# Kernel optimization log

Hardware: AMD Instinct MI355X
Metric: run time of the kernel (lower is better)

The kernel has to match this reference:

```python
import jax, jax.numpy as jnp
import numpy as np

H = 256          # hidden_channels
R = 64           # num_rbf
N = 20000        # nodes
E = 320000       # edges
CUTOFF_LO = 0.0
CUTOFF_UP = 5.0
LN_EPS = 1e-5


def _layernorm(x, g, b):
    mu = jnp.mean(x, axis=-1, keepdims=True)
    var = jnp.var(x, axis=-1, keepdims=True)
    return (x - mu) * jax.lax.rsqrt(var + LN_EPS) * g + b


def _cosine_cutoff(r):
    # cutoff_lower == 0 branch of CosineCutoff
    c = 0.5 * (jnp.cos(r * (jnp.pi / CUTOFF_UP)) + 1.0)
    return c * (r < CUTOFF_UP).astype(r.dtype)


def setup_inputs() -> dict:
    key = jax.random.key(0)
    ks = jax.random.split(key, 16)
    def xavier(k, shape):
        fan_in, fan_out = shape[1], shape[0]
        lim = np.sqrt(6.0 / (fan_in + fan_out))
        return jax.random.uniform(k, shape, jnp.float32, -lim, lim)
    x = jax.random.normal(ks[0], (N, H), jnp.float32)
    edge_index = jax.random.randint(ks[1], (2, E), 0, N, jnp.int64)
    edge_weight = jax.random.uniform(ks[2], (E,), jnp.float32, 0.0, CUTOFF_UP)
    edge_attr = jax.random.normal(ks[3], (E, R), jnp.float32)
    return {
        "x": x,
        "edge_index": edge_index,
        "edge_weight": edge_weight,
        "edge_attr": edge_attr,
        "ln_g": jnp.ones((H,), jnp.float32),
        "ln_b": jnp.zeros((H,), jnp.float32),
        "Wq": xavier(ks[4], (H, H)), "bq": jnp.zeros((H,), jnp.float32),
        "Wk": xavier(ks[5], (H, H)), "bk": jnp.zeros((H,), jnp.float32),
        "Wv": xavier(ks[6], (H, H)), "bv": jnp.zeros((H,), jnp.float32),
        "Wo": xavier(ks[7], (H, H)), "bo": jnp.zeros((H,), jnp.float32),
        "Wdk": xavier(ks[8], (H, R)), "bdk": jnp.zeros((H,), jnp.float32),
        "Wdv": xavier(ks[9], (H, R)), "bdv": jnp.zeros((H,), jnp.float32),
    }


def reference(x, edge_index, edge_weight, edge_attr,
              ln_g, ln_b, Wq, bq, Wk, bk, Wv, bv, Wo, bo, Wdk, bdk, Wdv, bdv):
    src = edge_index[0]  # j (messages come from)
    dst = edge_index[1]  # i (messages aggregate to)

    x_norm = _layernorm(x, ln_g, ln_b)                     # [N,H]
    q = x_norm @ Wq.T + bq                                 # [N,H]
    k = x_norm @ Wk.T + bk
    v = x_norm @ Wv.T + bv

    dk = jax.nn.silu(edge_attr @ Wdk.T + bdk)              # [E,H]
    dv = jax.nn.silu(edge_attr @ Wdv.T + bdv)              # [E,H]

    q_i = q[dst]                                           # [E,H]
    k_j = k[src]
    v_j = v[src]

    attn = jnp.sum(q_i * k_j * dk, axis=1)                 # [E]
    attn = jax.nn.silu(attn) * _cosine_cutoff(edge_weight) # [E]

    msg = v_j * dv * attn[:, None]                         # [E,H]
    agg = jax.ops.segment_sum(msg, dst, num_segments=x.shape[0])  # [N,H]

    out = agg @ Wo.T + bo
    return x + out
```

## Files before the change

kernel.cpp:

```cpp
#include <hip/hip_runtime.h>
#include <math.h>

#define NN 20000
#define H 256
#define R 64
#define EE 320000
#define LN_EPS 1e-5f
#define NB 79

using short8  = __attribute__((ext_vector_type(8))) short;
using ushort8 = __attribute__((ext_vector_type(8))) unsigned short;
using f32x4   = __attribute__((ext_vector_type(4))) float;

typedef __attribute__((address_space(3))) unsigned int lds_uint;
typedef const __attribute__((address_space(1))) unsigned int glb_uint;

__device__ __forceinline__ float silu_f(float x) { return x / (1.0f + __expf(-x)); }

__device__ __forceinline__ unsigned short f2bf(float f) {
    unsigned u = __float_as_uint(f);
    u += 0x7fff + ((u >> 16) & 1);
    return (unsigned short)(u >> 16);
}
__device__ __forceinline__ float bf2f(unsigned short s) {
    return __uint_as_float(((unsigned)s) << 16);
}

__device__ __forceinline__ int sw_idx(int row, int col) {
    return row * 64 + ((((col >> 3) ^ (row & 7)) << 3) | (col & 7));
}
__device__ __forceinline__ int dk_idx(int row, int col) {
    return row * 128 + (col ^ (((row >> 2) & 1) << 4));
}

__global__ __launch_bounds__(256) void k_prep(
    const float* __restrict__ Wq, const float* __restrict__ Wk,
    const float* __restrict__ Wv, const float* __restrict__ Wo,
    const float* __restrict__ g,  const float* __restrict__ b,
    const float* __restrict__ bq, const float* __restrict__ bk, const float* __restrict__ bv,
    const float* __restrict__ Wdk, const float* __restrict__ Wdv,
    unsigned short* __restrict__ wqkv_p, unsigned short* __restrict__ wo_p,
    unsigned short* __restrict__ wdk_p,  unsigned short* __restrict__ wdv_p,
    float* __restrict__ bias3)
{
    const int bid = blockIdx.x, t = threadIdx.x;
    if (bid < 128) {
        const int mat = bid >> 5;
        const float* W = mat == 0 ? Wq : (mat == 1 ? Wk : (mat == 2 ? Wv : Wo));
        unsigned short* out = (mat < 3) ? wqkv_p + (size_t)mat * 131072 : wo_p;
        const int fold = mat < 3;
        const int flat = (bid & 31) * 256 + t;
        const int tile = flat >> 9;
        const int rem  = flat & 511;
        const int ks   = rem >> 6;
        const int lane = rem & 63;
        const int nl = lane & 15, quad = lane >> 4;
        const int h  = tile * 16 + nl;
        const int c0 = ks * 32 + quad * 8;
        short8 hi8, lo8;
        #pragma unroll
        for (int j = 0; j < 8; ++j) {
            float wv = W[(size_t)h * 256 + c0 + j];
            if (fold) wv *= g[c0 + j];
            const unsigned short hh = f2bf(wv);
            hi8[j] = (short)hh;
            lo8[j] = (short)f2bf(wv - bf2f(hh));
        }
        unsigned short* ob = out + ((size_t)(tile * 8 + ks)) * 1024;
        *(short8*)&ob[lane * 8] = hi8;
        *(short8*)&ob[512 + lane * 8] = lo8;
    } else if (bid < 160) {
        const int flat = (bid - 128) * 256 + t;
        const int mat  = flat >> 12;
        const int rem  = flat & 4095;
        const int hh   = rem >> 11;
        const int r2   = rem & 2047;
        const int row  = r2 >> 4;
        const int col4 = (r2 & 15) * 4;
        const float* W = mat == 0 ? Wdk : Wdv;
        unsigned short* out = (mat == 0 ? wdk_p : wdv_p) + hh * 16384;
        const float4 w4 = *(const float4*)(W + (size_t)(hh * 128 + row) * 64 + col4);
        const unsigned short h0 = f2bf(w4.x), h1 = f2bf(w4.y), h2 = f2bf(w4.z), h3 = f2bf(w4.w);
        ushort4 hi4 = {h0, h1, h2, h3};
        ushort4 lo4 = {f2bf(w4.x - bf2f(h0)), f2bf(w4.y - bf2f(h1)),
                       f2bf(w4.z - bf2f(h2)), f2bf(w4.w - bf2f(h3))};
        const int di = sw_idx(row, col4);
        *(ushort4*)&out[di] = hi4;
        *(ushort4*)&out[8192 + di] = lo4;
    } else {
        const int mat = bid - 160, h = t;
        const float* W  = mat == 0 ? Wq : (mat == 1 ? Wk : Wv);
        const float* bb = mat == 0 ? bq : (mat == 1 ? bk : bv);
        float s = 0.f;
        const float* wr = W + (size_t)h * 256;
        for (int c = 0; c < 256; c += 4) {
            const float4 w4 = *(const float4*)(wr + c);
            const float4 b4 = *(const float4*)(b + c);
            s += w4.x * b4.x + w4.y * b4.y + w4.z * b4.z + w4.w * b4.w;
        }
        bias3[mat * 256 + h] = bb[h] + s;
    }
}

__global__ __launch_bounds__(64, 2) void k_ln_qkv(
    const float* __restrict__ x,
    const unsigned short* __restrict__ wqkv_p, const float* __restrict__ bias3,
    float* __restrict__ q, float* __restrict__ k, float* __restrict__ v)
{
    const int t = threadIdx.x;
    const int lane = t & 63;
    const int nl = lane & 15, quad = lane >> 4;
    const int nbase = blockIdx.x * 16;
    const int node = nbase + nl;
    const bool nv = node < NN;

    float xv[64];
    float sum = 0.f, sq = 0.f;
    {
        const float* xp = x + (size_t)node * H + quad * 8;
        #pragma unroll
        for (int ks = 0; ks < 8; ++ks) {
            float4 x0 = {0.f,0.f,0.f,0.f}, x1 = {0.f,0.f,0.f,0.f};
            if (nv) {
                x0 = *(const float4*)(xp + ks * 32);
                x1 = *(const float4*)(xp + ks * 32 + 4);
            }
            xv[ks*8+0]=x0.x; xv[ks*8+1]=x0.y; xv[ks*8+2]=x0.z; xv[ks*8+3]=x0.w;
            xv[ks*8+4]=x1.x; xv[ks*8+5]=x1.y; xv[ks*8+6]=x1.z; xv[ks*8+7]=x1.w;
            sum += x0.x+x0.y+x0.z+x0.w + x1.x+x1.y+x1.z+x1.w;
            sq  += x0.x*x0.x+x0.y*x0.y+x0.z*x0.z+x0.w*x0.w
                 + x1.x*x1.x+x1.y*x1.y+x1.z*x1.z+x1.w*x1.w;
        }
    }
    sum += __shfl_xor(sum, 16); sum += __shfl_xor(sum, 32);
    sq  += __shfl_xor(sq, 16);  sq  += __shfl_xor(sq, 32);
    const float mu  = sum * (1.0f / H);
    const float var = sq * (1.0f / H) - mu * mu;
    const float rs  = rsqrtf(var + LN_EPS);

    short8 a_hi[8], a_lo[8];
    #pragma unroll
    for (int ks = 0; ks < 8; ++ks) {
        #pragma unroll
        for (int j = 0; j < 8; ++j) {
            const float z = (xv[ks*8+j] - mu) * rs;
            const unsigned short hh = f2bf(z);
            a_hi[ks][j] = (short)hh;
            a_lo[ks][j] = (short)f2bf(z - bf2f(hh));
        }
    }

    for (int mat = 0; mat < 3; ++mat) {
        float* outp = mat == 0 ? q : (mat == 1 ? k : v);
        const float* bp = bias3 + mat * 256;
        const unsigned short* wb = wqkv_p + (size_t)mat * 131072 + lane * 8;
        for (int tile = 0; tile < 16; ++tile) {
            const unsigned short* gb = wb + (size_t)tile * 8192;
            const float bbv = bp[tile * 16 + nl];
            f32x4 acc = {bbv, bbv, bbv, bbv};
            #pragma unroll
            for (int ks = 0; ks < 8; ++ks) {
                const short8 b_hi = *(const short8*)(gb + ks * 1024);
                const short8 b_lo = *(const short8*)(gb + ks * 1024 + 512);
                acc = __builtin_amdgcn_mfma_f32_16x16x32_bf16(a_hi[ks], b_hi, acc, 0, 0, 0);
                acc = __builtin_amdgcn_mfma_f32_16x16x32_bf16(a_lo[ks], b_hi, acc, 0, 0, 0);
                acc = __builtin_amdgcn_mfma_f32_16x16x32_bf16(a_hi[ks], b_lo, acc, 0, 0, 0);
            }
            #pragma unroll
            for (int r = 0; r < 4; ++r) {
                const int onode = nbase + quad * 4 + r;
                if (onode < NN)
                    outp[(size_t)onode * H + tile * 16 + nl] = acc[r];
            }
        }
    }
}

__global__ __launch_bounds__(256) void k_hist(const int* __restrict__ ei, int* __restrict__ hist) {
    int e = blockIdx.x * 256 + threadIdx.x;
    if (e < EE) atomicAdd(&hist[ei[EE + e]], 1);
}

__global__ __launch_bounds__(256) void k_scan1(const int* __restrict__ hist,
                                               int* __restrict__ cursor, int* __restrict__ bsum) {
    const int t = threadIdx.x, i = blockIdx.x * 256 + t;
    const int lane = t & 63, w = t >> 6;
    const int v = (i < NN) ? hist[i] : 0;
    int incl = v;
    #pragma unroll
    for (int off = 1; off < 64; off <<= 1) {
        int u = __shfl_up(incl, off);
        if (lane >= off) incl += u;
    }
    __shared__ int ws[4];
    if (lane == 63) ws[w] = incl;
    __syncthreads();
    int base = 0;
    #pragma unroll
    for (int j = 0; j < 4; ++j) if (j < w) base += ws[j];
    if (i < NN) cursor[i] = base + incl - v;
    if (t == 255) bsum[blockIdx.x] = base + incl;
}

__global__ __launch_bounds__(128) void k_scan2(int* __restrict__ bsum) {
    __shared__ int buf[128];
    const int t = threadIdx.x;
    const int v = (t < NB) ? bsum[t] : 0;
    buf[t] = v;
    __syncthreads();
    #pragma unroll
    for (int off = 1; off < 128; off <<= 1) {
        int add = (t >= off) ? buf[t - off] : 0;
        __syncthreads();
        buf[t] += add;
        __syncthreads();
    }
    if (t < NB) bsum[t] = buf[t] - v;
}

__global__ __launch_bounds__(256) void k_scan3(int* __restrict__ cursor, const int* __restrict__ bsum) {
    const int i = blockIdx.x * 256 + threadIdx.x;
    if (i < NN) cursor[i] += bsum[blockIdx.x];
}

__global__ __launch_bounds__(256) void k_scatter(const int* __restrict__ ei,
                                                 int* __restrict__ cursor, int* __restrict__ perm) {
    int e = blockIdx.x * 256 + threadIdx.x;
    if (e < EE) {
        int d = ei[EE + e];
        int pos = atomicAdd(&cursor[d], 1);
        perm[pos] = e;
    }
}

__global__ __launch_bounds__(256, 4) void k_edge(
    const float* __restrict__ q, const float* __restrict__ k, const float* __restrict__ v,
    const int* __restrict__ ei, const float* __restrict__ ew, const float* __restrict__ ea,
    const unsigned short* __restrict__ wdk_p, const float* __restrict__ bdk,
    const unsigned short* __restrict__ wdv_p, const float* __restrict__ bdv,
    const int* __restrict__ perm,
    float* __restrict__ agg)
{
    __shared__ __align__(16) unsigned short w_region[2 * 128 * 64];
    __shared__ float attn_s[64];
    __shared__ int src_s[64], dst_s[64];

    unsigned short* w_hi_s = w_region;
    unsigned short* w_lo_s = w_region + 128 * 64;
    float* dks = (float*)w_region;

    const int t    = threadIdx.x;
    const int bi   = blockIdx.x;
    const int eb   = ((bi & 7) * 625 + (bi >> 3)) * 64;
    const int lane = t & 63, wave = t >> 6;
    const int nl   = lane & 15, quad = lane >> 4;
    const int estrip = wave * 16;
    const int tx = t & 31, ty = t >> 5;
    const int h0 = tx * 4, e0 = ty * 8;

    if (t < 64) {
        const int e = perm[eb + t];
        src_s[t] = ei[e];
        dst_s[t] = ei[EE + e];
        attn_s[t] = 0.f;
    }

    short8 a_hi[2], a_lo[2];
    {
        const int e = perm[eb + estrip + nl];
        const float* ap = ea + (size_t)e * R + quad * 8;
        #pragma unroll
        for (int ks = 0; ks < 2; ++ks) {
            const float4 x0 = *(const float4*)(ap + ks * 32);
            const float4 x1 = *(const float4*)(ap + ks * 32 + 4);
            const float zz[8] = {x0.x, x0.y, x0.z, x0.w, x1.x, x1.y, x1.z, x1.w};
            #pragma unroll
            for (int j = 0; j < 8; ++j) {
                const unsigned short hv = f2bf(zz[j]);
                a_hi[ks][j] = (short)hv;
                a_lo[ks][j] = (short)f2bf(zz[j] - bf2f(hv));
            }
        }
    }

    for (int hh = 0; hh < 2; ++hh) {
        __syncthreads();
        {
            const ushort8* sp = (const ushort8*)(wdk_p + (size_t)hh * 16384) + t;
            ushort8* dpw = (ushort8*)w_region + (t & 192);
            #pragma unroll
            for (int c = 0; c < 8; ++c)
                __builtin_amdgcn_global_load_lds((glb_uint*)(sp + c * 256),
                                                 (lds_uint*)(dpw + c * 256), 16, 0, 0);
        }
        __syncthreads();

        f32x4 accA[8];
        #pragma unroll
        for (int tt = 0; tt < 8; ++tt) {
            const int wrow = tt * 16 + nl;
            const int hcol = hh * 128 + tt * 16 + nl;
            short8 b_hi[2], b_lo[2];
            #pragma unroll
            for (int ks = 0; ks < 2; ++ks) {
                const int idx = wrow * 64 + ((((ks * 4 + quad) ^ (nl & 7)) << 3));
                b_hi[ks] = *(const short8*)&w_hi_s[idx];
                b_lo[ks] = *(const short8*)&w_lo_s[idx];
            }
            const float bb = bdk[hcol];
            f32x4 acc = {bb, bb, bb, bb};
            #pragma unroll
            for (int ks = 0; ks < 2; ++ks) {
                acc = __builtin_amdgcn_mfma_f32_16x16x32_bf16(a_hi[ks], b_hi[ks], acc, 0, 0, 0);
                acc = __builtin_amdgcn_mfma_f32_16x16x32_bf16(a_lo[ks], b_hi[ks], acc, 0, 0, 0);
                acc = __builtin_amdgcn_mfma_f32_16x16x32_bf16(a_hi[ks], b_lo[ks], acc, 0, 0, 0);
            }
            accA[tt] = acc;
        }
        __syncthreads();
        #pragma unroll
        for (int tt = 0; tt < 8; ++tt)
            #pragma unroll
            for (int r = 0; r < 4; ++r)
                dks[dk_idx(estrip + quad * 4 + r, tt * 16 + nl)] = silu_f(accA[tt][r]);
        __syncthreads();

        #pragma unroll
        for (int i = 0; i < 8; ++i) {
            const int d = dst_s[e0 + i], s = src_s[e0 + i];
            const float4 qi  = *(const float4*)(q + (size_t)d * H + hh * 128 + h0);
            const float4 kj  = *(const float4*)(k + (size_t)s * H + hh * 128 + h0);
            const float4 dk4 = *(const float4*)&dks[dk_idx(e0 + i, h0)];
            float part = qi.x * kj.x * dk4.x + qi.y * kj.y * dk4.y
                       + qi.z * kj.z * dk4.z + qi.w * kj.w * dk4.w;
            #pragma unroll
            for (int off = 16; off; off >>= 1) part += __shfl_xor(part, off);
            if (tx == 0) attn_s[e0 + i] += part;
        }
    }
    __syncthreads();
    if (t < 64) {
        const int e = perm[eb + t];
        const float rr = ew[e];
        const float cut = (rr < 5.0f) ? 0.5f * (__cosf(rr * 0.6283185307f) + 1.0f) : 0.0f;
        attn_s[t] = silu_f(attn_s[t]) * cut;
    }

    for (int hh = 0; hh < 2; ++hh) {
        __syncthreads();
        {
            const ushort8* sp = (const ushort8*)(wdv_p + (size_t)hh * 16384) + t;
            ushort8* dpw = (ushort8*)w_region + (t & 192);
            #pragma unroll
            for (int c = 0; c < 8; ++c)
                __builtin_amdgcn_global_load_lds((glb_uint*)(sp + c * 256),
                                                 (lds_uint*)(dpw + c * 256), 16, 0, 0);
        }
        __syncthreads();

        f32x4 accA[8];
        #pragma unroll
        for (int tt = 0; tt < 8; ++tt) {
            const int wrow = tt * 16 + nl;
            const int hcol = hh * 128 + tt * 16 + nl;
            short8 b_hi[2], b_lo[2];
            #pragma unroll
            for (int ks = 0; ks < 2; ++ks) {
                const int idx = wrow * 64 + ((((ks * 4 + quad) ^ (nl & 7)) << 3));
                b_hi[ks] = *(const short8*)&w_hi_s[idx];
                b_lo[ks] = *(const short8*)&w_lo_s[idx];
            }
            const float bb = bdv[hcol];
            f32x4 acc = {bb, bb, bb, bb};
            #pragma unroll
            for (int ks = 0; ks < 2; ++ks) {
                acc = __builtin_amdgcn_mfma_f32_16x16x32_bf16(a_hi[ks], b_hi[ks], acc, 0, 0, 0);
                acc = __builtin_amdgcn_mfma_f32_16x16x32_bf16(a_lo[ks], b_hi[ks], acc, 0, 0, 0);
                acc = __builtin_amdgcn_mfma_f32_16x16x32_bf16(a_hi[ks], b_lo[ks], acc, 0, 0, 0);
            }
            accA[tt] = acc;
        }
        __syncthreads();
        #pragma unroll
        for (int tt = 0; tt < 8; ++tt)
            #pragma unroll
            for (int r = 0; r < 4; ++r)
                dks[dk_idx(estrip + quad * 4 + r, tt * 16 + nl)] = silu_f(accA[tt][r]);
        __syncthreads();

        float4 m = {0.f, 0.f, 0.f, 0.f};
        int cur_d = -1;
        #pragma unroll
        for (int i = 0; i < 8; ++i) {
            const int d = dst_s[e0 + i], s = src_s[e0 + i];
            const float a = attn_s[e0 + i];
            const float4 vj  = *(const float4*)(v + (size_t)s * H + hh * 128 + h0);
            const float4 dv4 = *(const float4*)&dks[dk_idx(e0 + i, h0)];
            float4 mi;
            mi.x = vj.x * dv4.x * a;
            mi.y = vj.y * dv4.y * a;
            mi.z = vj.z * dv4.z * a;
            mi.w = vj.w * dv4.w * a;
            if (d != cur_d) {
                if (cur_d >= 0) {
                    float* dp = agg + (size_t)cur_d * H + hh * 128 + h0;
                    atomicAdd(dp + 0, m.x); atomicAdd(dp + 1, m.y);
                    atomicAdd(dp + 2, m.z); atomicAdd(dp + 3, m.w);
                }
                m = mi; cur_d = d;
            } else {
                m.x += mi.x; m.y += mi.y; m.z += mi.z; m.w += mi.w;
            }
        }
        {
            float* dp = agg + (size_t)cur_d * H + hh * 128 + h0;
            atomicAdd(dp + 0, m.x); atomicAdd(dp + 1, m.y);
            atomicAdd(dp + 2, m.z); atomicAdd(dp + 3, m.w);
        }
    }
}

__global__ __launch_bounds__(64, 2) void k_out(
    const float* __restrict__ aggm, const unsigned short* __restrict__ wo_p,
    const float* __restrict__ bo, const float* __restrict__ x, float* __restrict__ out)
{
    const int t = threadIdx.x;
    const int lane = t & 63;
    const int nl = lane & 15, quad = lane >> 4;
    const int nbase = blockIdx.x * 16;
    const int node = nbase + nl;
    const bool nv = node < NN;

    short8 a_hi[8], a_lo[8];
    {
        const float* ap = aggm + (size_t)node * H + quad * 8;
        #pragma unroll
        for (int ks = 0; ks < 8; ++ks) {
            float4 x0 = {0.f,0.f,0.f,0.f}, x1 = {0.f,0.f,0.f,0.f};
            if (nv) { x0 = *(const float4*)(ap + ks * 32); x1 = *(const float4*)(ap + ks * 32 + 4); }
            const float zz[8] = {x0.x,x0.y,x0.z,x0.w,x1.x,x1.y,x1.z,x1.w};
            #pragma unroll
            for (int j = 0; j < 8; ++j) {
                const unsigned short hh = f2bf(zz[j]);
                a_hi[ks][j] = (short)hh;
                a_lo[ks][j] = (short)f2bf(zz[j] - bf2f(hh));
            }
        }
    }
    for (int tile = 0; tile < 16; ++tile) {
        const unsigned short* gb = wo_p + (size_t)tile * 8192 + lane * 8;
        const float bbv = bo[tile * 16 + nl];
        f32x4 acc = {bbv, bbv, bbv, bbv};
        #pragma unroll
        for (int ks = 0; ks < 8; ++ks) {
            const short8 b_hi = *(const short8*)(gb + ks * 1024);
            const short8 b_lo = *(const short8*)(gb + ks * 1024 + 512);
            acc = __builtin_amdgcn_mfma_f32_16x16x32_bf16(a_hi[ks], b_hi, acc, 0, 0, 0);
            acc = __builtin_amdgcn_mfma_f32_16x16x32_bf16(a_lo[ks], b_hi, acc, 0, 0, 0);
            acc = __builtin_amdgcn_mfma_f32_16x16x32_bf16(a_hi[ks], b_lo, acc, 0, 0, 0);
        }
        #pragma unroll
        for (int r = 0; r < 4; ++r) {
            const int onode = nbase + quad * 4 + r;
            if (onode < NN) {
                const size_t oi = (size_t)onode * H + tile * 16 + nl;
                out[oi] = x[oi] + acc[r];
            }
        }
    }
}

extern "C" void kernel_launch(void* const* d_in, const int* in_sizes, int n_in,
                              void* d_out, int out_size, void* d_ws, size_t ws_size,
                              hipStream_t stream) {
    const float* x   = (const float*)d_in[0];
    const int*   ei  = (const int*)d_in[1];
    const float* ew  = (const float*)d_in[2];
    const float* ea  = (const float*)d_in[3];
    const float* g   = (const float*)d_in[4];
    const float* b   = (const float*)d_in[5];
    const float* Wq  = (const float*)d_in[6];  const float* bq  = (const float*)d_in[7];
    const float* Wk  = (const float*)d_in[8];  const float* bk  = (const float*)d_in[9];
    const float* Wv  = (const float*)d_in[10]; const float* bv  = (const float*)d_in[11];
    const float* Wo  = (const float*)d_in[12]; const float* bo  = (const float*)d_in[13];
    const float* Wdk = (const float*)d_in[14]; const float* bdk = (const float*)d_in[15];
    const float* Wdv = (const float*)d_in[16]; const float* bdv = (const float*)d_in[17];

    float* q    = (float*)d_ws;
    float* k    = q + (size_t)NN * H;
    float* v    = k + (size_t)NN * H;
    float* agg  = v + (size_t)NN * H;
    int*   hist = (int*)(agg + (size_t)NN * H);
    int*   cur  = hist + NN;
    int*   bsum = cur + NN;
    int*   perm = bsum + 128;
    unsigned short* wqkv_p = (unsigned short*)(perm + EE);
    unsigned short* wo_p   = wqkv_p + 393216;
    unsigned short* wdk_p  = wo_p + 131072;
    unsigned short* wdv_p  = wdk_p + 32768;
    float* bias3 = (float*)(wdv_p + 32768);

    hipMemsetAsync(hist, 0, NN * sizeof(int), stream);
    hipMemsetAsync(agg, 0, (size_t)NN * H * sizeof(float), stream);
    k_prep<<<163, 256, 0, stream>>>(Wq, Wk, Wv, Wo, g, b, bq, bk, bv, Wdk, Wdv,
                                    wqkv_p, wo_p, wdk_p, wdv_p, bias3);
    k_hist<<<EE / 256, 256, 0, stream>>>(ei, hist);
    k_ln_qkv<<<(NN + 15) / 16, 64, 0, stream>>>(x, wqkv_p, bias3, q, k, v);
    k_scan1<<<NB, 256, 0, stream>>>(hist, cur, bsum);
    k_scan2<<<1, 128, 0, stream>>>(bsum);
    k_scan3<<<NB, 256, 0, stream>>>(cur, bsum);
    k_scatter<<<EE / 256, 256, 0, stream>>>(ei, cur, perm);
    k_edge<<<EE / 64, 256, 0, stream>>>(q, k, v, ei, ew, ea, wdk_p, bdk, wdv_p, bdv, perm, agg);
    k_out<<<(NN + 15) / 16, 64, 0, stream>>>(agg, wo_p, bo, x, (float*)d_out);
}
```

Measured before the change: 651.3 us.

## Pipeline edge-kernel weight loads, store filter activations as fp16, fold scan and memset

The edge kernel's four GEMM phases (dk halves, dv halves) become one loop. The next weight half is prefetched into LDS via global_load_lds while the current silu outputs are written to a separate fp16 LDS buffer, which removes barriers and overlaps the load latency. The silu division becomes a hardware reciprocal. The hist memset moves into k_prep, and k_scan3 is folded into k_scatter by adding the block offset there, which saves launches. The fp16 filter storage lowers precision, and the added LDS buffer cuts occupancy (launch bounds drop from 4 to 3).

```diff
diff --git a/kernel.cpp b/kernel.cpp
--- a/kernel.cpp
+++ b/kernel.cpp
@@ -15,7 +15,9 @@
 typedef __attribute__((address_space(3))) unsigned int lds_uint;
 typedef const __attribute__((address_space(1))) unsigned int glb_uint;
 
-__device__ __forceinline__ float silu_f(float x) { return x / (1.0f + __expf(-x)); }
+__device__ __forceinline__ float silu_f(float x) {
+    return x * __builtin_amdgcn_rcpf(1.0f + __expf(-x));
+}
 
 __device__ __forceinline__ unsigned short f2bf(float f) {
     unsigned u = __float_as_uint(f);
@@ -25,12 +27,22 @@
 __device__ __forceinline__ float bf2f(unsigned short s) {
     return __uint_as_float(((unsigned)s) << 16);
 }
+__device__ __forceinline__ unsigned short f2h(float f) {
+    unsigned r;
+    asm("v_cvt_f16_f32 %0, %1" : "=v"(r) : "v"(f));
+    return (unsigned short)r;
+}
+__device__ __forceinline__ float h2f(unsigned short h) {
+    float f;
+    asm("v_cvt_f32_f16 %0, %1" : "=v"(f) : "v"((unsigned)h));
+    return f;
+}
 
 __device__ __forceinline__ int sw_idx(int row, int col) {
     return row * 64 + ((((col >> 3) ^ (row & 7)) << 3) | (col & 7));
 }
-__device__ __forceinline__ int dk_idx(int row, int col) {
-    return row * 128 + (col ^ (((row >> 2) & 1) << 4));
+__device__ __forceinline__ int dh_idx(int row, int col) {
+    return row * 128 + (col ^ (((row >> 2) & 3) << 4));
 }
 
 __global__ __launch_bounds__(256) void k_prep(
@@ -41,7 +53,7 @@
     const float* __restrict__ Wdk, const float* __restrict__ Wdv,
     unsigned short* __restrict__ wqkv_p, unsigned short* __restrict__ wo_p,
     unsigned short* __restrict__ wdk_p,  unsigned short* __restrict__ wdv_p,
-    float* __restrict__ bias3)
+    float* __restrict__ bias3, int* __restrict__ hist)
 {
     const int bid = blockIdx.x, t = threadIdx.x;
     if (bid < 128) {
@@ -87,7 +99,7 @@
         const int di = sw_idx(row, col4);
         *(ushort4*)&out[di] = hi4;
         *(ushort4*)&out[8192 + di] = lo4;
-    } else {
+    } else if (bid < 163) {
         const int mat = bid - 160, h = t;
         const float* W  = mat == 0 ? Wq : (mat == 1 ? Wk : Wv);
         const float* bb = mat == 0 ? bq : (mat == 1 ? bk : bv);
@@ -99,6 +111,9 @@
             s += w4.x * b4.x + w4.y * b4.y + w4.z * b4.z + w4.w * b4.w;
         }
         bias3[mat * 256 + h] = bb[h] + s;
+    } else {
+        const int i = (bid - 163) * 256 + t;
+        if (i < NN) hist[i] = 0;
     }
 }
 
@@ -218,22 +233,19 @@
     if (t < NB) bsum[t] = buf[t] - v;
 }
 
-__global__ __launch_bounds__(256) void k_scan3(int* __restrict__ cursor, const int* __restrict__ bsum) {
-    const int i = blockIdx.x * 256 + threadIdx.x;
-    if (i < NN) cursor[i] += bsum[blockIdx.x];
-}
-
 __global__ __launch_bounds__(256) void k_scatter(const int* __restrict__ ei,
-                                                 int* __restrict__ cursor, int* __restrict__ perm) {
+                                                 int* __restrict__ cursor,
+                                                 const int* __restrict__ bsum,
+                                                 int* __restrict__ perm) {
     int e = blockIdx.x * 256 + threadIdx.x;
     if (e < EE) {
         int d = ei[EE + e];
-        int pos = atomicAdd(&cursor[d], 1);
+        int pos = atomicAdd(&cursor[d], 1) + bsum[d >> 8];
         perm[pos] = e;
     }
 }
 
-__global__ __launch_bounds__(256, 4) void k_edge(
+__global__ __launch_bounds__(256, 3) void k_edge(
     const float* __restrict__ q, const float* __restrict__ k, const float* __restrict__ v,
     const int* __restrict__ ei, const float* __restrict__ ew, const float* __restrict__ ea,
     const unsigned short* __restrict__ wdk_p, const float* __restrict__ bdk,
@@ -242,12 +254,12 @@
     float* __restrict__ agg)
 {
     __shared__ __align__(16) unsigned short w_region[2 * 128 * 64];
+    __shared__ __align__(16) unsigned short dks_h[64 * 128];
     __shared__ float attn_s[64];
     __shared__ int src_s[64], dst_s[64];
 
-    unsigned short* w_hi_s = w_region;
-    unsigned short* w_lo_s = w_region + 128 * 64;
-    float* dks = (float*)w_region;
+    const unsigned short* w_hi_s = w_region;
+    const unsigned short* w_lo_s = w_region + 128 * 64;
 
     const int t    = threadIdx.x;
     const int bi   = blockIdx.x;
@@ -258,6 +270,15 @@
     const int tx = t & 31, ty = t >> 5;
     const int h0 = tx * 4, e0 = ty * 8;
 
+    {
+        const ushort8* sp = (const ushort8*)wdk_p + t;
+        ushort8* dpw = (ushort8*)w_region + (t & 192);
+        #pragma unroll
+        for (int c = 0; c < 8; ++c)
+            __builtin_amdgcn_global_load_lds((glb_uint*)(sp + c * 256),
+                                             (lds_uint*)(dpw + c * 256), 16, 0, 0);
+    }
+
     if (t < 64) {
         const int e = perm[eb + t];
         src_s[t] = ei[e];
@@ -282,24 +303,23 @@
             }
         }
     }
-
-    for (int hh = 0; hh < 2; ++hh) {
-        __syncthreads();
-        {
-            const ushort8* sp = (const ushort8*)(wdk_p + (size_t)hh * 16384) + t;
-            ushort8* dpw = (ushort8*)w_region + (t & 192);
-            #pragma unroll
-            for (int c = 0; c < 8; ++c)
-                __builtin_amdgcn_global_load_lds((glb_uint*)(sp + c * 256),
-                                                 (lds_uint*)(dpw + c * 256), 16, 0, 0);
-        }
-        __syncthreads();
-
+    __syncthreads();
+
+    for (int img = 0; img < 4; ++img) {
+        const int hh = img & 1;
+
+        if (img == 2 && t < 64) {
+            const int e = perm[eb + t];
+            const float rr = ew[e];
+            const float cut = (rr < 5.0f) ? 0.5f * (__cosf(rr * 0.6283185307f) + 1.0f) : 0.0f;
+            attn_s[t] = silu_f(attn_s[t]) * cut;
+        }
+
+        const float* bias = (img < 2) ? bdk : bdv;
         f32x4 accA[8];
         #pragma unroll
         for (int tt = 0; tt < 8; ++tt) {
             const int wrow = tt * 16 + nl;
-            const int hcol = hh * 128 + tt * 16 + nl;
             short8 b_hi[2], b_lo[2];
             #pragma unroll
             for (int ks = 0; ks < 2; ++ks) {
@@ -307,7 +327,7 @@
                 b_hi[ks] = *(const short8*)&w_hi_s[idx];
                 b_lo[ks] = *(const short8*)&w_lo_s[idx];
             }
-            const float bb = bdk[hcol];
+            const float bb = bias[hh * 128 + tt * 16 + nl];
             f32x4 acc = {bb, bb, bb, bb};
             #pragma unroll
             for (int ks = 0; ks < 2; ++ks) {
@@ -318,105 +338,70 @@
             accA[tt] = acc;
         }
         __syncthreads();
-        #pragma unroll
-        for (int tt = 0; tt < 8; ++tt)
-            #pragma unroll
-            for (int r = 0; r < 4; ++r)
-                dks[dk_idx(estrip + quad * 4 + r, tt * 16 + nl)] = silu_f(accA[tt][r]);
-        __syncthreads();
-
-        #pragma unroll
-        for (int i = 0; i < 8; ++i) {
-            const int d = dst_s[e0 + i], s = src_s[e0 + i];
-            const float4 qi  = *(const float4*)(q + (size_t)d * H + hh * 128 + h0);
-            const float4 kj  = *(const float4*)(k + (size_t)s * H + hh * 128 + h0);
-            const float4 dk4 = *(const float4*)&dks[dk_idx(e0 + i, h0)];
-            float part = qi.x * kj.x * dk4.x + qi.y * kj.y * dk4.y
-                       + qi.z * kj.z * dk4.z + qi.w * kj.w * dk4.w;
-            #pragma unroll
-            for (int off = 16; off; off >>= 1) part += __shfl_xor(part, off);
-            if (tx == 0) attn_s[e0 + i] += part;
-        }
-    }
-    __syncthreads();
-    if (t < 64) {
-        const int e = perm[eb + t];
-        const float rr = ew[e];
-        const float cut = (rr < 5.0f) ? 0.5f * (__cosf(rr * 0.6283185307f) + 1.0f) : 0.0f;
-        attn_s[t] = silu_f(attn_s[t]) * cut;
-    }
-
-    for (int hh = 0; hh < 2; ++hh) {
-        __syncthreads();
-        {
-            const ushort8* sp = (const ushort8*)(wdv_p + (size_t)hh * 16384) + t;
+
+        if (img < 3) {
+            const unsigned short* nip = (img == 0) ? wdk_p + 16384
+                                      : (img == 1) ? wdv_p : wdv_p + 16384;
+            const ushort8* sp = (const ushort8*)nip + t;
             ushort8* dpw = (ushort8*)w_region + (t & 192);
             #pragma unroll
             for (int c = 0; c < 8; ++c)
                 __builtin_amdgcn_global_load_lds((glb_uint*)(sp + c * 256),
                                                  (lds_uint*)(dpw + c * 256), 16, 0, 0);
         }
+
+        #pragma unroll
+        for (int tt = 0; tt < 8; ++tt)
+            #pragma unroll
+            for (int r = 0; r < 4; ++r)
+                dks_h[dh_idx(estrip + quad * 4 + r, tt * 16 + nl)] =
+                    f2h(silu_f(accA[tt][r]));
+
+        if (img < 2) {
+            #pragma unroll
+            for (int i = 0; i < 8; ++i) {
+                const int d = dst_s[e0 + i], s = src_s[e0 + i];
+                const float4 qi = *(const float4*)(q + (size_t)d * H + hh * 128 + h0);
+                const float4 kj = *(const float4*)(k + (size_t)s * H + hh * 128 + h0);
+                const ushort4 dk4 = *(const ushort4*)&dks_h[dh_idx(e0 + i, h0)];
+                float part = qi.x * kj.x * h2f(dk4.x) + qi.y * kj.y * h2f(dk4.y)
+                           + qi.z * kj.z * h2f(dk4.z) + qi.w * kj.w * h2f(dk4.w);
+                #pragma unroll
+                for (int off = 16; off; off >>= 1) part += __shfl_xor(part, off);
+                if (tx == 0) attn_s[e0 + i] += part;
+            }
+        } else {
+            float4 m = {0.f, 0.f, 0.f, 0.f};
+            int cur_d = -1;
+            #pragma unroll
+            for (int i = 0; i < 8; ++i) {
+                const int d = dst_s[e0 + i], s = src_s[e0 + i];
+                const float a = attn_s[e0 + i];
+                const float4 vj = *(const float4*)(v + (size_t)s * H + hh * 128 + h0);
+                const ushort4 dv4 = *(const ushort4*)&dks_h[dh_idx(e0 + i, h0)];
+                float4 mi;
+                mi.x = vj.x * h2f(dv4.x) * a;
+                mi.y = vj.y * h2f(dv4.y) * a;
+                mi.z = vj.z * h2f(dv4.z) * a;
+                mi.w = vj.w * h2f(dv4.w) * a;
+                if (d != cur_d) {
+                    if (cur_d >= 0) {
+                        float* dp = agg + (size_t)cur_d * H + hh * 128 + h0;
+                        atomicAdd(dp + 0, m.x); atomicAdd(dp + 1, m.y);
+                        atomicAdd(dp + 2, m.z); atomicAdd(dp + 3, m.w);
+                    }
+                    m = mi; cur_d = d;
+                } else {
+                    m.x += mi.x; m.y += mi.y; m.z += mi.z; m.w += mi.w;
+                }
+            }
+            {
+                float* dp = agg + (size_t)cur_d * H + hh * 128 + h0;
+                atomicAdd(dp + 0, m.x); atomicAdd(dp + 1, m.y);
+                atomicAdd(dp + 2, m.z); atomicAdd(dp + 3, m.w);
+            }
+        }
         __syncthreads();
-
-        f32x4 accA[8];
-        #pragma unroll
-        for (int tt = 0; tt < 8; ++tt) {
-            const int wrow = tt * 16 + nl;
-            const int hcol = hh * 128 + tt * 16 + nl;
-            short8 b_hi[2], b_lo[2];
-            #pragma unroll
-            for (int ks = 0; ks < 2; ++ks) {
-                const int idx = wrow * 64 + ((((ks * 4 + quad) ^ (nl & 7)) << 3));
-                b_hi[ks] = *(const short8*)&w_hi_s[idx];
-                b_lo[ks] = *(const short8*)&w_lo_s[idx];
-            }
-            const float bb = bdv[hcol];
-            f32x4 acc = {bb, bb, bb, bb};
-            #pragma unroll
-            for (int ks = 0; ks < 2; ++ks) {
-                acc = __builtin_amdgcn_mfma_f32_16x16x32_bf16(a_hi[ks], b_hi[ks], acc, 0, 0, 0);
-                acc = __builtin_amdgcn_mfma_f32_16x16x32_bf16(a_lo[ks], b_hi[ks], acc, 0, 0, 0);
-                acc = __builtin_amdgcn_mfma_f32_16x16x32_bf16(a_hi[ks], b_lo[ks], acc, 0, 0, 0);
-            }
-            accA[tt] = acc;
-        }
-        __syncthreads();
-        #pragma unroll
-        for (int tt = 0; tt < 8; ++tt)
-            #pragma unroll
-            for (int r = 0; r < 4; ++r)
-                dks[dk_idx(estrip + quad * 4 + r, tt * 16 + nl)] = silu_f(accA[tt][r]);
-        __syncthreads();
-
-        float4 m = {0.f, 0.f, 0.f, 0.f};
-        int cur_d = -1;
-        #pragma unroll
-        for (int i = 0; i < 8; ++i) {
-            const int d = dst_s[e0 + i], s = src_s[e0 + i];
-            const float a = attn_s[e0 + i];
-            const float4 vj  = *(const float4*)(v + (size_t)s * H + hh * 128 + h0);
-            const float4 dv4 = *(const float4*)&dks[dk_idx(e0 + i, h0)];
-            float4 mi;
-            mi.x = vj.x * dv4.x * a;
-            mi.y = vj.y * dv4.y * a;
-            mi.z = vj.z * dv4.z * a;
-            mi.w = vj.w * dv4.w * a;
-            if (d != cur_d) {
-                if (cur_d >= 0) {
-                    float* dp = agg + (size_t)cur_d * H + hh * 128 + h0;
-                    atomicAdd(dp + 0, m.x); atomicAdd(dp + 1, m.y);
-                    atomicAdd(dp + 2, m.z); atomicAdd(dp + 3, m.w);
-                }
-                m = mi; cur_d = d;
-            } else {
-                m.x += mi.x; m.y += mi.y; m.z += mi.z; m.w += mi.w;
-            }
-        }
-        {
-            float* dp = agg + (size_t)cur_d * H + hh * 128 + h0;
-            atomicAdd(dp + 0, m.x); atomicAdd(dp + 1, m.y);
-            atomicAdd(dp + 2, m.z); atomicAdd(dp + 3, m.w);
-        }
     }
 }
 
@@ -500,16 +485,14 @@
     unsigned short* wdv_p  = wdk_p + 32768;
     float* bias3 = (float*)(wdv_p + 32768);
 
-    hipMemsetAsync(hist, 0, NN * sizeof(int), stream);
     hipMemsetAsync(agg, 0, (size_t)NN * H * sizeof(float), stream);
-    k_prep<<<163, 256, 0, stream>>>(Wq, Wk, Wv, Wo, g, b, bq, bk, bv, Wdk, Wdv,
-                                    wqkv_p, wo_p, wdk_p, wdv_p, bias3);
+    k_prep<<<242, 256, 0, stream>>>(Wq, Wk, Wv, Wo, g, b, bq, bk, bv, Wdk, Wdv,
+                                    wqkv_p, wo_p, wdk_p, wdv_p, bias3, hist);
     k_hist<<<EE / 256, 256, 0, stream>>>(ei, hist);
     k_ln_qkv<<<(NN + 15) / 16, 64, 0, stream>>>(x, wqkv_p, bias3, q, k, v);
     k_scan1<<<NB, 256, 0, stream>>>(hist, cur, bsum);
     k_scan2<<<1, 128, 0, stream>>>(bsum);
-    k_scan3<<<NB, 256, 0, stream>>>(cur, bsum);
-    k_scatter<<<EE / 256, 256, 0, stream>>>(ei, cur, perm);
+    k_scatter<<<EE / 256, 256, 0, stream>>>(ei, cur, bsum, perm);
     k_edge<<<EE / 64, 256, 0, stream>>>(q, k, v, ei, ew, ea, wdk_p, bdk, wdv_p, bdv, perm, agg);
     k_out<<<(NN + 15) / 16, 64, 0, stream>>>(agg, wo_p, bo, x, (float*)d_out);
 }
```

New measurement: 647.8 us. About the same (-0.5%).
